# Kernel tuning notes

Hardware: AMD Instinct MI355X
Metric: run time of the kernel (lower is better)

Reference implementation:

```python
import jax, jax.numpy as jnp
import numpy as np

B, T = 16, 64
IN, H = 256, 512          # input_size, hidden_size (= output_size)
M, W, R = 256, 64, 4      # nr_cells, cell_size, read_heads
NN_IN = R * W + IN        # controller input size = 512
IFACE = R * W + 3 * W + 5 * R + 3  # 471
DELTA = 1e-6


def _lin(key, fan_out, fan_in):
    k1, k2 = jax.random.split(key)
    s = 1.0 / np.sqrt(fan_in)
    Wm = jax.random.uniform(k1, (fan_out, fan_in), minval=-s, maxval=s, dtype=jnp.float32)
    b = jax.random.uniform(k2, (fan_out,), minval=-s, maxval=s, dtype=jnp.float32)
    return Wm, b


def setup_inputs() -> dict:
    key = jax.random.key(0)
    ks = jax.random.split(key, 8)
    x = jax.random.normal(ks[0], (B, T, IN), dtype=jnp.float32)
    Wih0, bih0 = _lin(ks[1], 4 * H, NN_IN)
    Whh0, bhh0 = _lin(ks[2], 4 * H, H)
    Wih1, bih1 = _lin(ks[3], 4 * H, H)
    Whh1, bhh1 = _lin(ks[4], 4 * H, H)
    Wout, bout = _lin(ks[5], H, H)              # output_weights
    Wif, bif = _lin(ks[6], IFACE, H)            # memory interface_weights
    Wmem, bmem = _lin(ks[7], IN, R * W + H)     # mem_out
    return dict(x=x, Wih0=Wih0, bih0=bih0, Whh0=Whh0, bhh0=bhh0,
                Wih1=Wih1, bih1=bih1, Whh1=Whh1, bhh1=bhh1,
                Wout=Wout, bout=bout, Wif=Wif, bif=bif, Wmem=Wmem, bmem=bmem)


def _lstm(x, h, c, Wih, bih, Whh, bhh):
    g = x @ Wih.T + bih + h @ Whh.T + bhh
    i, f, gg, o = jnp.split(g, 4, axis=-1)  # torch LSTMCell gate order i,f,g,o
    i, f, o = jax.nn.sigmoid(i), jax.nn.sigmoid(f), jax.nn.sigmoid(o)
    c = f * c + i * jnp.tanh(gg)
    return o * jnp.tanh(c), c


def _content_weights(mem, keys, strengths):
    # mem (B,M,W), keys (B,K,W), strengths (B,K) -> softmax cosine weights (B,K,M)
    mn = mem / (jnp.linalg.norm(mem, axis=2, keepdims=True) + DELTA)
    kn = keys / (jnp.linalg.norm(keys, axis=2, keepdims=True) + DELTA)
    sim = jnp.einsum('bkw,bmw->bkm', kn, mn)
    return jax.nn.softmax(sim * strengths[:, :, None], axis=2)


def _dnc_forward(x, Wih0, bih0, Whh0, bhh0, Wih1, bih1, Whh1, bhh1,
                 Wout, bout, Wif, bif, Wmem, bmem):
    Bz, Tz = x.shape[0], x.shape[1]
    eye_mask = 1.0 - jnp.eye(M, dtype=x.dtype)
    # NOTE: in the source, last_read (zeros at init) is concatenated to EVERY
    # timestep's input and never updated inside the layer time loop.
    last_read = jnp.zeros((Bz, Tz, R * W), dtype=x.dtype)
    xs = jnp.swapaxes(jnp.concatenate([x, last_read], axis=-1), 0, 1)  # (T,B,NN_IN)

    def step(carry, xt):
        h0, c0, h1, c1, mem, link, prec, rw, ww, usage = carry
        h0, c0 = _lstm(xt, h0, c0, Wih0, bih0, Whh0, bhh0)
        h1, c1 = _lstm(h0, h1, c1, Wih1, bih1, Whh1, bhh1)
        out = h1 @ Wout.T + bout
        xi = h1 @ Wif.T + bif  # (B, IFACE)
        o1 = R * W
        rk = jnp.tanh(xi[:, :o1]).reshape(Bz, R, W)
        rs = jax.nn.softplus(xi[:, o1:o1 + R])
        o2 = o1 + R
        wk = jnp.tanh(xi[:, o2:o2 + W]).reshape(Bz, 1, W)
        ws = jax.nn.softplus(xi[:, o2 + W:o2 + W + 1])          # (B,1)
        ev = jax.nn.sigmoid(xi[:, o2 + W + 1:o2 + 2 * W + 1])   # erase (B,W)
        wv = jnp.tanh(xi[:, o2 + 2 * W + 1:o2 + 3 * W + 1])     # write vec (B,W)
        o3 = o2 + 3 * W + 1
        fg = jax.nn.sigmoid(xi[:, o3:o3 + R])                   # free gates (B,R)
        ag = jax.nn.sigmoid(xi[:, o3 + R:o3 + R + 1])           # alloc gate (B,1)
        wg = jax.nn.sigmoid(xi[:, o3 + R + 1:o3 + R + 2])       # write gate (B,1)
        rm = jax.nn.softmax(xi[:, o3 + R + 2:].reshape(Bz, R, 3), axis=-1)
        # --- usage update (single write head: 1 - prod(1-ww) == ww) ---
        usage = usage + (1.0 - usage) * ww
        psi = jnp.prod(1.0 - fg[:, :, None] * rw, axis=1)
        usage = usage * psi
        # --- write content weighting ---
        wcw = _content_weights(mem, wk, ws)[:, 0]  # (B,M)
        # --- allocation via sort + exclusive cumprod + inverse scatter ---
        u = DELTA + (1.0 - DELTA) * usage
        idx = jnp.argsort(u, axis=1)  # ascending usage = free list
        su = jnp.take_along_axis(u, idx, axis=1)
        prod_excl = jnp.cumprod(jnp.concatenate([jnp.ones((Bz, 1), u.dtype), su], 1), axis=1)[:, :-1]
        sa = (1.0 - su) * prod_excl
        alloc = jnp.take_along_axis(sa, jnp.argsort(idx, axis=1), axis=1)  # (B,M)
        # --- write weighting ---
        ww = wg * (ag * alloc + (1.0 - ag) * wcw)  # (B,M)
        # --- memory erase + write ---
        mem = mem * (1.0 - ww[:, :, None] * ev[:, None, :]) + ww[:, :, None] * wv[:, None, :]
        # --- temporal link matrix (diag zeroed) + precedence ---
        link = (1.0 - ww[:, :, None] - ww[:, None, :]) * link + ww[:, :, None] * prec[:, None, :]
        link = link * eye_mask
        prec = (1.0 - jnp.sum(ww, axis=1, keepdims=True)) * prec + ww
        # --- read: content + forward/backward directional modes ---
        cw = _content_weights(mem, rk, rs)            # (B,R,M)
        fwd = jnp.einsum('bmn,brn->brm', link, rw)    # L @ rw_prev
        bwd = jnp.einsum('brm,bmn->brn', rw, link)    # rw_prev @ L
        rw = rm[:, :, 0:1] * bwd + rm[:, :, 1:2] * fwd + rm[:, :, 2:3] * cw
        read_vecs = jnp.einsum('brm,bmw->brw', rw, mem).reshape(Bz, R * W)
        y = jnp.concatenate([out, read_vecs], axis=1) @ Wmem.T + bmem  # mem_out, dropout=0
        return (h0, c0, h1, c1, mem, link, prec, rw, ww, usage), y

    z = lambda *s: jnp.zeros(s, dtype=x.dtype)
    init = (z(Bz, H), z(Bz, H), z(Bz, H), z(Bz, H),
            z(Bz, M, W), z(Bz, M, M), z(Bz, M), z(Bz, R, M), z(Bz, M), z(Bz, M))
    _, ys = jax.lax.scan(step, init, xs)
    return jnp.swapaxes(ys, 0, 1)  # (B,T,IN)


def reference(x, Wih0, bih0, Whh0, bhh0, Wih1, bih1, Whh1, bhh1,
              Wout, bout, Wif, bif, Wmem, bmem):
    return _dnc_forward(x, Wih0, bih0, Whh0, bhh0, Wih1, bih1, Whh1, bhh1,
                        Wout, bout, Wif, bif, Wmem, bmem)
```

## Files before the change

kernel.cpp:

```cpp
#include <hip/hip_runtime.h>
#include <math.h>


#define BZ    16
#define TZ    64
#define HID   512
#define NCELL 256
#define CSZ   64
#define NRD   4
#define G4H   2048
#define IFC   471
#define DEL   1e-6f
#define SMT   257
#define NLSTM 192
#define NTOT  224

__device__ __forceinline__ float sig_(float x) { return 1.f / (1.f + expf(-x)); }
__device__ __forceinline__ float splus_(float x) { return fmaxf(x, 0.f) + log1pf(expf(-fabsf(x))); }

template <int SLP>
__device__ __forceinline__ unsigned poll_acq(unsigned* ptr, unsigned tgt) {
  unsigned v;
  while ((v = __hip_atomic_load(ptr, __ATOMIC_RELAXED, __HIP_MEMORY_SCOPE_AGENT)) < tgt)
    __builtin_amdgcn_s_sleep(SLP);
  v = __hip_atomic_load(ptr, __ATOMIC_ACQUIRE, __HIP_MEMORY_SCOPE_AGENT);
  return v;
}

__global__ __launch_bounds__(256) void k_transpose(const float* __restrict__ src,
                                                   float* __restrict__ dst,
                                                   int rows, int cols, int kmax, int dst_stride) {
  __shared__ float tile[32][33];
  int c0 = blockIdx.x * 32, r0 = blockIdx.y * 32;
  int tx = threadIdx.x, ty = threadIdx.y;
  for (int i = ty; i < 32; i += 8) {
    int r = r0 + i, c = c0 + tx;
    tile[i][tx] = (r < rows && c < cols) ? src[(size_t)r * cols + c] : 0.f;
  }
  __syncthreads();
  for (int i = ty; i < 32; i += 8) {
    int c = c0 + i, r = r0 + tx;
    if (c < kmax && r < rows) dst[(size_t)c * dst_stride + r] = tile[tx][i];
  }
}

__global__ __launch_bounds__(256) void k_xpart(const float* __restrict__ x,
                                               const float* __restrict__ Wih0T,
                                               const float* __restrict__ bih0,
                                               const float* __restrict__ bhh0,
                                               float* __restrict__ xpart) {
  const int lane = threadIdx.x, ty = threadIdx.y;
  const int jg = blockIdx.x * 64 + lane;
  const int tb0 = blockIdx.y * 16;
  __shared__ float sx[16][256];
  const int tid = ty * 64 + lane;
  for (int idx = tid; idx < 16 * 256; idx += 256) {
    int row = idx >> 8, k = idx & 255;
    int tb = tb0 + row, tt = tb >> 4, bb = tb & 15;
    sx[row][k] = x[((size_t)bb * TZ + tt) * 256 + k];
  }
  __syncthreads();
  float acc[4] = {0.f, 0.f, 0.f, 0.f};
  for (int k = 0; k < 256; ++k) {
    float wv = Wih0T[(size_t)k * G4H + jg];
#pragma unroll
    for (int i = 0; i < 4; ++i) acc[i] = fmaf(wv, sx[ty * 4 + i][k], acc[i]);
  }
  float bias = bih0[jg] + bhh0[jg];
#pragma unroll
  for (int i = 0; i < 4; ++i)
    xpart[(size_t)(tb0 + ty * 4 + i) * G4H + jg] = acc[i] + bias;
}

__device__ __forceinline__ void gbar(unsigned* done, unsigned* go,
                                     unsigned tgt, int bid, int tid) {
  __syncthreads();
  if (bid == 0) {
    if (tid == 0)
      __hip_atomic_store(&done[0], tgt, __ATOMIC_RELEASE, __HIP_MEMORY_SCOPE_AGENT);
    if (tid < NLSTM) (void)poll_acq<4>(&done[tid], tgt);
    __syncthreads();
    if (tid == 0)
      __hip_atomic_store(go, tgt, __ATOMIC_RELEASE, __HIP_MEMORY_SCOPE_AGENT);
  } else {
    if (tid == 0) {
      __hip_atomic_store(&done[bid], tgt, __ATOMIC_RELEASE, __HIP_MEMORY_SCOPE_AGENT);
      (void)poll_acq<4>(go, tgt);
    }
    __syncthreads();
  }
}

#define SCR(s, i) scr[(s) * 1320 + (i)]

__global__ __launch_bounds__(1024, 1) void k_fused(
    const float* __restrict__ xpart,
    const float* __restrict__ Whh0,
    const float* __restrict__ Wih1, const float* __restrict__ Whh1,
    const float* __restrict__ bih1, const float* __restrict__ bhh1,
    const float* __restrict__ WifT, const float* __restrict__ bif,
    float* __restrict__ h0g, float* __restrict__ h1g,
    float* __restrict__ h1_all, float* __restrict__ xi_all,
    float* __restrict__ linkg, float* __restrict__ rv_all,
    unsigned* __restrict__ done, unsigned* __restrict__ go,
    unsigned* __restrict__ xiflag) {
  const int tid = threadIdx.x;
  const int bid = blockIdx.x;
  __shared__ __align__(16) float SMEM[37264];

  if (bid < 64) {
    float* w0 = SMEM;
    float* hl = SMEM + 16768;
    float* sc = hl + 8320;
    float* xpl = sc + 4096;
    float* c0l = xpl + 512;
    const int j0 = bid * 8;
    for (int lr = 0; lr < 32; ++lr) {
      int g = lr >> 3, jj2 = lr & 7;
      const float* src = Whh0 + (size_t)(g * 512 + j0 + jj2) * 512;
      for (int k = tid; k < 512; k += 1024) w0[lr * 524 + k] = src[k];
    }
    if (tid < 128) c0l[tid] = 0.f;
    const int ks = tid & 7, bq = (tid >> 3) & 3, jj = tid >> 5;
    const int wr0 = (0 * 8 + (jj & 7)) * 524, wr1 = (1 * 8 + (jj & 7)) * 524,
              wr2 = (2 * 8 + (jj & 7)) * 524, wr3 = (3 * 8 + (jj & 7)) * 524;
    const int hb0 = (bq * 4 + 0) * 520, hb1 = (bq * 4 + 1) * 520,
              hb2 = (bq * 4 + 2) * 520, hb3 = (bq * 4 + 3) * 520;
    for (int ph = 0; ph < 65; ++ph) {
      if (ph < 64) {
        const int t = ph, po = t & 1, pn = po ^ 1;
        for (int q = tid; q < 2048; q += 1024) {
          int bb = q >> 7, kq = q & 127;
          ((float4*)&hl[bb * 520])[kq] = ((const float4*)&h0g[(size_t)(po * 16 + bb) * 512])[kq];
        }
        if (tid < 512) {
          int bb = tid >> 5, g = (tid >> 3) & 3, j2 = tid & 7;
          xpl[tid] = xpart[((size_t)t * 16 + bb) * G4H + g * 512 + j0 + j2];
        }
        __syncthreads();
        if (tid < 256) {
          float4 a0 = {0,0,0,0}, a1 = {0,0,0,0}, a2 = {0,0,0,0}, a3 = {0,0,0,0};
#pragma unroll 4
          for (int i = 0; i < 16; ++i) {
            const int off = ks * 4 + 32 * i;
            float4 w4a = *(const float4*)&w0[wr0 + off];
            float4 w4b = *(const float4*)&w0[wr1 + off];
            float4 w4c = *(const float4*)&w0[wr2 + off];
            float4 w4d = *(const float4*)&w0[wr3 + off];
            float4 h4a = *(const float4*)&hl[hb0 + off];
            float4 h4b = *(const float4*)&hl[hb1 + off];
            float4 h4c = *(const float4*)&hl[hb2 + off];
            float4 h4d = *(const float4*)&hl[hb3 + off];
            a0.x += w4a.x*h4a.x + w4a.y*h4a.y + w4a.z*h4a.z + w4a.w*h4a.w;
            a0.y += w4a.x*h4b.x + w4a.y*h4b.y + w4a.z*h4b.z + w4a.w*h4b.w;
            a0.z += w4a.x*h4c.x + w4a.y*h4c.y + w4a.z*h4c.z + w4a.w*h4c.w;
            a0.w += w4a.x*h4d.x + w4a.y*h4d.y + w4a.z*h4d.z + w4a.w*h4d.w;
            a1.x += w4b.x*h4a.x + w4b.y*h4a.y + w4b.z*h4a.z + w4b.w*h4a.w;
            a1.y += w4b.x*h4b.x + w4b.y*h4b.y + w4b.z*h4b.z + w4b.w*h4b.w;
            a1.z += w4b.x*h4c.x + w4b.y*h4c.y + w4b.z*h4c.z + w4b.w*h4c.w;
            a1.w += w4b.x*h4d.x + w4b.y*h4d.y + w4b.z*h4d.z + w4b.w*h4d.w;
            a2.x += w4c.x*h4a.x + w4c.y*h4a.y + w4c.z*h4a.z + w4c.w*h4a.w;
            a2.y += w4c.x*h4b.x + w4c.y*h4b.y + w4c.z*h4b.z + w4c.w*h4b.w;
            a2.z += w4c.x*h4c.x + w4c.y*h4c.y + w4c.z*h4c.z + w4c.w*h4c.w;
            a2.w += w4c.x*h4d.x + w4c.y*h4d.y + w4c.z*h4d.z + w4c.w*h4d.w;
            a3.x += w4d.x*h4a.x + w4d.y*h4a.y + w4d.z*h4a.z + w4d.w*h4a.w;
            a3.y += w4d.x*h4b.x + w4d.y*h4b.y + w4d.z*h4b.z + w4d.w*h4b.w;
            a3.z += w4d.x*h4c.x + w4d.y*h4c.y + w4d.z*h4c.z + w4d.w*h4c.w;
            a3.w += w4d.x*h4d.x + w4d.y*h4d.y + w4d.z*h4d.z + w4d.w*h4d.w;
          }
          *(float4*)&sc[ks * 512 + (0 * 8 + jj) * 16 + bq * 4] = a0;
          *(float4*)&sc[ks * 512 + (1 * 8 + jj) * 16 + bq * 4] = a1;
          *(float4*)&sc[ks * 512 + (2 * 8 + jj) * 16 + bq * 4] = a2;
          *(float4*)&sc[ks * 512 + (3 * 8 + jj) * 16 + bq * 4] = a3;
        }
        __syncthreads();
        if (tid < 128) {
          const int bb = tid >> 3, j2 = tid & 7;
          float gs[4];
#pragma unroll
          for (int g = 0; g < 4; ++g) {
            float s = 0.f;
#pragma unroll
            for (int k2 = 0; k2 < 8; ++k2) s += sc[k2 * 512 + (g * 8 + j2) * 16 + bb];
            gs[g] = s + xpl[bb * 32 + g * 8 + j2];
          }
          float gi = sig_(gs[0]), gf = sig_(gs[1]), gg = tanhf(gs[2]), go_ = sig_(gs[3]);
          float cc = gf * c0l[j2 * 16 + bb] + gi * gg;
          c0l[j2 * 16 + bb] = cc;
          h0g[(size_t)(pn * 16 + bb) * 512 + j0 + j2] = go_ * tanhf(cc);
        }
      }
      gbar(done, go, (unsigned)(ph + 1), bid, tid);
    }
  } else if (bid < 192) {
    float* w1 = SMEM;
    float* h0l = SMEM + 16448;
    float* h1l = h0l + 8320;
    float* sc = h1l + 8320;
    float* c1l = sc + 4096;
    float* bl = c1l + 64;
    const int b1 = bid - 64;
    const int j0 = b1 * 4;
    for (int lr = 0; lr < 16; ++lr) {
      int g = lr >> 2, jj2 = lr & 3;
      const float* si = Wih1 + (size_t)(g * 512 + j0 + jj2) * 512;
      const float* sh = Whh1 + (size_t)(g * 512 + j0 + jj2) * 512;
      for (int k = tid; k < 512; k += 1024) {
        w1[lr * 1028 + k] = si[k];
        w1[lr * 1028 + 512 + k] = sh[k];
      }
    }
    if (tid < 64) c1l[tid] = 0.f;
    if (tid < 16) {
      int g = tid >> 2, jj2 = tid & 3;
      bl[tid] = bih1[g * 512 + j0 + jj2] + bhh1[g * 512 + j0 + jj2];
    }
    const int ks = tid & 15, bq = (tid >> 4) & 3, jj = (tid >> 6) & 3;
    const int wr0 = (0 * 4 + jj) * 1028, wr1 = (1 * 4 + jj) * 1028,
              wr2 = (2 * 4 + jj) * 1028, wr3 = (3 * 4 + jj) * 1028;
    const int hb0 = (bq * 4 + 0) * 520, hb1 = (bq * 4 + 1) * 520,
              hb2 = (bq * 4 + 2) * 520, hb3 = (bq * 4 + 3) * 520;
    for (int ph = 0; ph < 65; ++ph) {
      if (ph >= 1) {
        const int t = ph - 1, po = t & 1, pn = po ^ 1;
        for (int q = tid; q < 2048; q += 1024) {
          int bb = q >> 7, kq = q & 127;
          ((float4*)&h0l[bb * 520])[kq] = ((const float4*)&h0g[(size_t)(pn * 16 + bb) * 512])[kq];
          ((float4*)&h1l[bb * 520])[kq] = ((const float4*)&h1g[(size_t)(po * 16 + bb) * 512])[kq];
        }
        __syncthreads();
        if (tid < 256) {
          float4 a0 = {0,0,0,0}, a1 = {0,0,0,0}, a2 = {0,0,0,0}, a3 = {0,0,0,0};
#pragma unroll 4
          for (int i = 0; i < 16; ++i) {
            const int offw = ks * 4 + 64 * i;
            const int offh = (i < 8) ? offw : (offw - 512);
            const float* hsrc = (i < 8) ? h0l : h1l;
            float4 w4a = *(const float4*)&w1[wr0 + offw];
            float4 w4b = *(const float4*)&w1[wr1 + offw];
            float4 w4c = *(const float4*)&w1[wr2 + offw];
            float4 w4d = *(const float4*)&w1[wr3 + offw];
            float4 h4a = *(const float4*)&hsrc[hb0 + offh];
            float4 h4b = *(const float4*)&hsrc[hb1 + offh];
            float4 h4c = *(const float4*)&hsrc[hb2 + offh];
            float4 h4d = *(const float4*)&hsrc[hb3 + offh];
            a0.x += w4a.x*h4a.x + w4a.y*h4a.y + w4a.z*h4a.z + w4a.w*h4a.w;
            a0.y += w4a.x*h4b.x + w4a.y*h4b.y + w4a.z*h4b.z + w4a.w*h4b.w;
            a0.z += w4a.x*h4c.x + w4a.y*h4c.y + w4a.z*h4c.z + w4a.w*h4c.w;
            a0.w += w4a.x*h4d.x + w4a.y*h4d.y + w4a.z*h4d.z + w4a.w*h4d.w;
            a1.x += w4b.x*h4a.x + w4b.y*h4a.y + w4b.z*h4a.z + w4b.w*h4a.w;
            a1.y += w4b.x*h4b.x + w4b.y*h4b.y + w4b.z*h4b.z + w4b.w*h4b.w;
            a1.z += w4b.x*h4c.x + w4b.y*h4c.y + w4b.z*h4c.z + w4b.w*h4c.w;
            a1.w += w4b.x*h4d.x + w4b.y*h4d.y + w4b.z*h4d.z + w4b.w*h4d.w;
            a2.x += w4c.x*h4a.x + w4c.y*h4a.y + w4c.z*h4a.z + w4c.w*h4a.w;
            a2.y += w4c.x*h4b.x + w4c.y*h4b.y + w4c.z*h4b.z + w4c.w*h4b.w;
            a2.z += w4c.x*h4c.x + w4c.y*h4c.y + w4c.z*h4c.z + w4c.w*h4c.w;
            a2.w += w4c.x*h4d.x + w4c.y*h4d.y + w4c.z*h4d.z + w4c.w*h4d.w;
            a3.x += w4d.x*h4a.x + w4d.y*h4a.y + w4d.z*h4a.z + w4d.w*h4a.w;
            a3.y += w4d.x*h4b.x + w4d.y*h4b.y + w4d.z*h4b.z + w4d.w*h4b.w;
            a3.z += w4d.x*h4c.x + w4d.y*h4c.y + w4d.z*h4c.z + w4d.w*h4c.w;
            a3.w += w4d.x*h4d.x + w4d.y*h4d.y + w4d.z*h4d.z + w4d.w*h4d.w;
          }
          *(float4*)&sc[ks * 256 + (0 * 4 + jj) * 16 + bq * 4] = a0;
          *(float4*)&sc[ks * 256 + (1 * 4 + jj) * 16 + bq * 4] = a1;
          *(float4*)&sc[ks * 256 + (2 * 4 + jj) * 16 + bq * 4] = a2;
          *(float4*)&sc[ks * 256 + (3 * 4 + jj) * 16 + bq * 4] = a3;
        }
        __syncthreads();
        if (tid < 64) {
          const int bb = tid >> 2, j2 = tid & 3;
          float gs[4];
#pragma unroll
          for (int g = 0; g < 4; ++g) {
            float s = 0.f;
#pragma unroll
            for (int k2 = 0; k2 < 16; ++k2) s += sc[k2 * 256 + (g * 4 + j2) * 16 + bb];
            gs[g] = s + bl[g * 4 + j2];
          }
          float gi = sig_(gs[0]), gf = sig_(gs[1]), gg = tanhf(gs[2]), go_ = sig_(gs[3]);
          float cc = gf * c1l[j2 * 16 + bb] + gi * gg;
          c1l[j2 * 16 + bb] = cc;
          float hv = go_ * tanhf(cc);
          h1g[(size_t)(pn * 16 + bb) * 512 + j0 + j2] = hv;
          h1_all[((size_t)t * 16 + bb) * 512 + j0 + j2] = hv;
        }
      }
      gbar(done, go, (unsigned)(ph + 1), bid, tid);
    }
  } else if (bid < 208) {
    const int b = bid - 192;
    float* sh1 = SMEM;
    float* sxo = SMEM + 512;
    __shared__ unsigned sgo;
    unsigned seen_go = 0;
    for (int t = 0; t < TZ; ++t) {
      if (tid == 0 && seen_go < (unsigned)(t + 2)) {
        sgo = poll_acq<8>(go, (unsigned)(t + 2));
      }
      __syncthreads();
      seen_go = (sgo > seen_go) ? sgo : seen_go;
      if (tid < 512) sh1[tid] = h1_all[((size_t)t * BZ + b) * HID + tid];
      __syncthreads();
      {
        const int u = tid & 511, half = tid >> 9;
        if (u < IFC) {
          const float* wc = WifT + u;
          const int k0 = half * 256;
          float acc = 0.f;
#pragma unroll 8
          for (int k = k0; k < k0 + 256; ++k)
            acc = fmaf(sh1[k], wc[(size_t)k * 512], acc);
          sxo[half * 512 + u] = acc;
        }
      }
      __syncthreads();
      if (tid < IFC)
        xi_all[((size_t)t * BZ + b) * 512 + tid] = sxo[tid] + sxo[512 + tid] + bif[tid];
      __syncthreads();
      if (tid == 0)
        __hip_atomic_store(&xiflag[b], (unsigned)(t + 1), __ATOMIC_RELEASE, __HIP_MEMORY_SCOPE_AGENT);
    }
  } else {
    const int b = bid - 208;
    const int lane = tid & 63;
    const int wv = tid >> 6;
    const int m8 = tid & 255;
    const int seg = tid >> 8;
    float* LNK = linkg + (size_t)b * (NCELL * NCELL);

    float* smemT = SMEM;
    float* sxi   = smemT + 16448;
    float* srkn  = sxi + 472;
    float* swkn  = srkn + 256;
    float* sev   = swkn + 64;
    float* swvv  = sev + 64;
    float* sscal = swvv + 64;
    float* srw   = sscal + 40;
    float* sww   = srw + 1024;
    float* susage = sww + 256;
    float* sprec = susage + 256;
    float* ssim  = sprec + 256;
    float* sfwd  = ssim + 1024;
    float* sbwd  = sfwd + 1024;
    float* sa    = sbwd + 1056;
    float* sc_   = sa + 256;
    float* sb_   = sc_ + 256;
    int*   srank = (int*)(sb_ + 256);
    float* scr   = (float*)(srank + 256);
    float* sred2 = scr + 5280;
    __shared__ unsigned sflag;

    for (int i = tid; i < CSZ * SMT; i += 1024) smemT[i] = 0.f;
    if (tid < 256) {
      sww[tid] = 0.f; susage[tid] = 0.f; sprec[tid] = 0.f;
      srw[tid] = 0.f; srw[256 + tid] = 0.f; srw[512 + tid] = 0.f; srw[768 + tid] = 0.f;
    }
    for (int i = tid; i < (NCELL * NCELL) / 4; i += 1024)
      ((float4*)LNK)[i] = make_float4(0.f, 0.f, 0.f, 0.f);
    __syncthreads();

    unsigned seen = 0;
    for (int t = 0; t < TZ; ++t) {
      if (tid == 0 && seen < (unsigned)(t + 1)) {
        sflag = poll_acq<8>(&xiflag[b], (unsigned)(t + 1));
      }
      __syncthreads();
      if (seen < (unsigned)(t + 1)) seen = sflag;

      if (tid < IFC) sxi[tid] = xi_all[((size_t)t * BZ + b) * 512 + tid];
      __syncthreads();
      if (wv < 4) {
        float v = tanhf(sxi[wv * 64 + lane]);
        float s2 = v * v;
#pragma unroll
        for (int off = 32; off; off >>= 1) s2 += __shfl_xor(s2, off);
        srkn[wv * 64 + lane] = v / (sqrtf(s2) + DEL);
      } else if (wv == 4) {
        float v = tanhf(sxi[260 + lane]);
        float s2 = v * v;
#pragma unroll
        for (int off = 32; off; off >>= 1) s2 += __shfl_xor(s2, off);
        swkn[lane] = v / (sqrtf(s2) + DEL);
      } else if (wv == 5) {
        sev[lane] = sig_(sxi[325 + lane]);
      } else if (wv == 6) {
        swvv[lane] = tanhf(sxi[389 + lane]);
      } else if (wv == 7) {
        if (lane < 4) sscal[lane] = splus_(sxi[256 + lane]);
        if (lane == 4) sscal[4] = splus_(sxi[324]);
        if (lane >= 8 && lane < 12) sscal[lane] = sig_(sxi[453 + (lane - 8)]);
        if (lane == 12) sscal[12] = sig_(sxi[457]);
        if (lane == 13) sscal[13] = sig_(sxi[458]);
        if (lane >= 16 && lane < 20) {
          int r = lane - 16;
          float a = sxi[459 + r * 3], b2 = sxi[460 + r * 3], c2 = sxi[461 + r * 3];
          float mx3 = fmaxf(a, fmaxf(b2, c2));
          float ea = expf(a - mx3), eb = expf(b2 - mx3), ec = expf(c2 - mx3);
          float iv = 1.f / (ea + eb + ec);
          sscal[20 + r * 3 + 0] = ea * iv;
          sscal[20 + r * 3 + 1] = eb * iv;
          sscal[20 + r * 3 + 2] = ec * iv;
        }
      }
      __syncthreads();

      float un_r = 0.f;
      if (tid < 256) {
        float wwo = sww[tid], uo = susage[tid];
        float u1 = uo + (1.f - uo) * wwo;
        float psi = 1.f;
#pragma unroll
        for (int r = 0; r < 4; ++r) psi *= 1.f - sscal[8 + r] * srw[r * 256 + tid];
        un_r = u1 * psi;
        susage[tid] = un_r;
      }
      {
        float dot = 0.f, nn = 0.f;
#pragma unroll 4
        for (int w = seg * 16; w < seg * 16 + 16; ++w) {
          float mv = smemT[w * SMT + m8];
          dot = fmaf(mv, swkn[w], dot);
          nn = fmaf(mv, mv, nn);
        }
        SCR(seg, 0 * 264 + m8) = dot;
        SCR(seg, 1 * 264 + m8) = nn;
      }
      __syncthreads();
      float e_r = 0.f, simv = 0.f;
      if (tid < 256) {
        float dot = SCR(0, tid) + SCR(1, tid) + SCR(2, tid) + SCR(3, tid);
        float nn = SCR(0, 264 + tid) + SCR(1, 264 + tid) + SCR(2, 264 + tid) + SCR(3, 264 + tid);
        simv = sscal[4] * dot / (sqrtf(nn) + DEL);
        float mx = simv;
#pragma unroll
        for (int off = 32; off; off >>= 1) mx = fmaxf(mx, __shfl_xor(mx, off));
        if (lane == 0) sred2[wv] = mx;
      }
      __syncthreads();
      if (tid < 256) {
        float mx = fmaxf(fmaxf(sred2[0], sred2[1]), fmaxf(sred2[2], sred2[3]));
        e_r = expf(simv - mx);
        float s = e_r;
#pragma unroll
        for (int off = 32; off; off >>= 1) s += __shfl_xor(s, off);
        if (lane == 0) sred2[8 + wv] = s;
      }
      __syncthreads();
      float wcw_r = 0.f;
      if (tid < 256) {
        float sm = sred2[8] + sred2[9] + sred2[10] + sred2[11];
        wcw_r = e_r / sm;
        sa[tid] = DEL + (1.f - DEL) * un_r;
      }
      __syncthreads();

      {
        float um = sa[m8];
        int cnt = 0;
        for (int j2 = seg * 64; j2 < seg * 64 + 64; ++j2) {
          float uj = sa[j2];
          cnt += (uj < um || (uj == um && j2 < m8)) ? 1 : 0;
        }
        ((int*)&SCR(seg, 0))[m8] = cnt;
      }
      __syncthreads();
      if (tid < 256) {
        int rank = ((int*)&SCR(0, 0))[tid] + ((int*)&SCR(1, 0))[tid] +
                   ((int*)&SCR(2, 0))[tid] + ((int*)&SCR(3, 0))[tid];
        srank[tid] = rank;
        sb_[rank] = sa[tid];
      }
      __syncthreads();
      float inc = 0.f;
      if (tid < 256) {
        inc = sb_[tid];
#pragma unroll
        for (int off = 1; off < 64; off <<= 1) {
          float pp = __shfl_up(inc, off);
          if (lane >= off) inc *= pp;
        }
        if (lane == 63) sred2[16 + wv] = inc;
      }
      __syncthreads();
      if (tid < 256) {
        float pref = 1.f;
        for (int w2 = 0; w2 < wv; ++w2) pref *= sred2[16 + w2];
        float excl = __shfl_up(inc, 1);
        if (lane == 0) excl = 1.f;
        sc_[tid] = excl * pref;
      }
      __syncthreads();

      if (tid < 256) {
        float alo = (1.f - sa[tid]) * sc_[srank[tid]];
        float wwn = sscal[13] * (sscal[12] * alo + (1.f - sscal[12]) * wcw_r);
        sww[tid] = wwn;
        float s = wwn;
#pragma unroll
        for (int off = 32; off; off >>= 1) s += __shfl_xor(s, off);
        if (lane == 0) sred2[24 + wv] = s;
      }
      __syncthreads();
      if (tid == 0) sscal[14] = sred2[24] + sred2[25] + sred2[26] + sred2[27];

      {
        float wm = sww[m8];
        float nn = 0.f, d0 = 0.f, d1 = 0.f, d2 = 0.f, d3 = 0.f;
#pragma unroll 4
        for (int w = seg * 16; w < seg * 16 + 16; ++w) {
          float v = smemT[w * SMT + m8];
          v = v * (1.f - wm * sev[w]) + wm * swvv[w];
          smemT[w * SMT + m8] = v;
          nn = fmaf(v, v, nn);
          d0 = fmaf(v, srkn[0 * 64 + w], d0);
          d1 = fmaf(v, srkn[1 * 64 + w], d1);
          d2 = fmaf(v, srkn[2 * 64 + w], d2);
          d3 = fmaf(v, srkn[3 * 64 + w], d3);
        }
        SCR(seg, 0 * 264 + m8) = nn;
        SCR(seg, 1 * 264 + m8) = d0;
        SCR(seg, 2 * 264 + m8) = d1;
        SCR(seg, 3 * 264 + m8) = d2;
        SCR(seg, 4 * 264 + m8) = d3;
      }
      for (int i = tid; i < NRD * 264; i += 1024) sbwd[i] = 0.f;
      __syncthreads();
      float sv0 = 0.f, sv1 = 0.f, sv2 = 0.f, sv3 = 0.f;
      float e0 = 0.f, e1 = 0.f, e2 = 0.f, e3 = 0.f;
      if (tid < 256) {
        float nn = SCR(0, tid) + SCR(1, tid) + SCR(2, tid) + SCR(3, tid);
        float invn = 1.f / (sqrtf(nn) + DEL);
        sv0 = sscal[0] * (SCR(0, 264 + tid) + SCR(1, 264 + tid) + SCR(2, 264 + tid) + SCR(3, 264 + tid)) * invn;
        sv1 = sscal[1] * (SCR(0, 528 + tid) + SCR(1, 528 + tid) + SCR(2, 528 + tid) + SCR(3, 528 + tid)) * invn;
        sv2 = sscal[2] * (SCR(0, 792 + tid) + SCR(1, 792 + tid) + SCR(2, 792 + tid) + SCR(3, 792 + tid)) * invn;
        sv3 = sscal[3] * (SCR(0, 1056 + tid) + SCR(1, 1056 + tid) + SCR(2, 1056 + tid) + SCR(3, 1056 + tid)) * invn;
        float m0 = sv0, m1 = sv1, m2 = sv2, m3 = sv3;
#pragma unroll
        for (int off = 32; off; off >>= 1) {
          m0 = fmaxf(m0, __shfl_xor(m0, off));
          m1 = fmaxf(m1, __shfl_xor(m1, off));
          m2 = fmaxf(m2, __shfl_xor(m2, off));
          m3 = fmaxf(m3, __shfl_xor(m3, off));
        }
        if (lane == 0) {
          sred2[wv * 4 + 0] = m0; sred2[wv * 4 + 1] = m1;
          sred2[wv * 4 + 2] = m2; sred2[wv * 4 + 3] = m3;
        }
      }
      __syncthreads();
      if (tid < 256) {
        float m0 = fmaxf(fmaxf(sred2[0], sred2[4]), fmaxf(sred2[8], sred2[12]));
        float m1 = fmaxf(fmaxf(sred2[1], sred2[5]), fmaxf(sred2[9], sred2[13]));
        float m2 = fmaxf(fmaxf(sred2[2], sred2[6]), fmaxf(sred2[10], sred2[14]));
        float m3 = fmaxf(fmaxf(sred2[3], sred2[7]), fmaxf(sred2[11], sred2[15]));
        e0 = expf(sv0 - m0); e1 = expf(sv1 - m1); e2 = expf(sv2 - m2); e3 = expf(sv3 - m3);
        float s0 = e0, s1 = e1, s2 = e2, s3 = e3;
#pragma unroll
        for (int off = 32; off; off >>= 1) {
          s0 += __shfl_xor(s0, off); s1 += __shfl_xor(s1, off);
          s2 += __shfl_xor(s2, off); s3 += __shfl_xor(s3, off);
        }
        if (lane == 0) {
          sred2[32 + wv * 4 + 0] = s0; sred2[32 + wv * 4 + 1] = s1;
          sred2[32 + wv * 4 + 2] = s2; sred2[32 + wv * 4 + 3] = s3;
        }
      }
      __syncthreads();
      if (tid < 256) {
        float s0 = sred2[32] + sred2[36] + sred2[40] + sred2[44];
        float s1 = sred2[33] + sred2[37] + sred2[41] + sred2[45];
        float s2 = sred2[34] + sred2[38] + sred2[42] + sred2[46];
        float s3 = sred2[35] + sred2[39] + sred2[43] + sred2[47];
        ssim[0 * 256 + tid] = e0 / s0; ssim[1 * 256 + tid] = e1 / s1;
        ssim[2 * 256 + tid] = e2 / s2; ssim[3 * 256 + tid] = e3 / s3;
      }

      {
        const float4 r0 = ((const float4*)(srw + 0 * 256))[lane];
        const float4 r1 = ((const float4*)(srw + 1 * 256))[lane];
        const float4 r2 = ((const float4*)(srw + 2 * 256))[lane];
        const float4 r3 = ((const float4*)(srw + 3 * 256))[lane];
        const float4 wc = ((const float4*)sww)[lane];
        const float4 pc = ((const float4*)sprec)[lane];
        const int n0 = lane * 4;
        float4 bp0 = {0,0,0,0}, bp1 = {0,0,0,0}, bp2 = {0,0,0,0}, bp3 = {0,0,0,0};
        for (int rr = 0; rr < 16; ++rr) {
          const int m = wv * 16 + rr;
          const float wm = sww[m];
          float4 lv = ((float4*)(LNK + (size_t)m * 256))[lane];
          lv.x = (1.f - wm - wc.x) * lv.x + wm * pc.x;
          lv.y = (1.f - wm - wc.y) * lv.y + wm * pc.y;
          lv.z = (1.f - wm - wc.z) * lv.z + wm * pc.z;
          lv.w = (1.f - wm - wc.w) * lv.w + wm * pc.w;
          if (m == n0 + 0) lv.x = 0.f;
          if (m == n0 + 1) lv.y = 0.f;
          if (m == n0 + 2) lv.z = 0.f;
          if (m == n0 + 3) lv.w = 0.f;
          ((float4*)(LNK + (size_t)m * 256))[lane] = lv;
          float f0 = lv.x * r0.x + lv.y * r0.y + lv.z * r0.z + lv.w * r0.w;
          float f1 = lv.x * r1.x + lv.y * r1.y + lv.z * r1.z + lv.w * r1.w;
          float f2 = lv.x * r2.x + lv.y * r2.y + lv.z * r2.z + lv.w * r2.w;
          float f3 = lv.x * r3.x + lv.y * r3.y + lv.z * r3.z + lv.w * r3.w;
#pragma unroll
          for (int off = 32; off; off >>= 1) {
            f0 += __shfl_xor(f0, off); f1 += __shfl_xor(f1, off);
            f2 += __shfl_xor(f2, off); f3 += __shfl_xor(f3, off);
          }
          if (lane == 0) {
            sfwd[0 * 256 + m] = f0; sfwd[1 * 256 + m] = f1;
            sfwd[2 * 256 + m] = f2; sfwd[3 * 256 + m] = f3;
          }
          const float s0 = srw[0 * 256 + m], s1 = srw[1 * 256 + m],
                      s2 = srw[2 * 256 + m], s3 = srw[3 * 256 + m];
          bp0.x = fmaf(lv.x, s0, bp0.x); bp0.y = fmaf(lv.y, s0, bp0.y);
          bp0.z = fmaf(lv.z, s0, bp0.z); bp0.w = fmaf(lv.w, s0, bp0.w);
          bp1.x = fmaf(lv.x, s1, bp1.x); bp1.y = fmaf(lv.y, s1, bp1.y);
          bp1.z = fmaf(lv.z, s1, bp1.z); bp1.w = fmaf(lv.w, s1, bp1.w);
          bp2.x = fmaf(lv.x, s2, bp2.x); bp2.y = fmaf(lv.y, s2, bp2.y);
          bp2.z = fmaf(lv.z, s2, bp2.z); bp2.w = fmaf(lv.w, s2, bp2.w);
          bp3.x = fmaf(lv.x, s3, bp3.x); bp3.y = fmaf(lv.y, s3, bp3.y);
          bp3.z = fmaf(lv.z, s3, bp3.z); bp3.w = fmaf(lv.w, s3, bp3.w);
        }
        atomicAdd(&sbwd[0 * 264 + n0 + 0], bp0.x); atomicAdd(&sbwd[0 * 264 + n0 + 1], bp0.y);
        atomicAdd(&sbwd[0 * 264 + n0 + 2], bp0.z); atomicAdd(&sbwd[0 * 264 + n0 + 3], bp0.w);
        atomicAdd(&sbwd[1 * 264 + n0 + 0], bp1.x); atomicAdd(&sbwd[1 * 264 + n0 + 1], bp1.y);
        atomicAdd(&sbwd[1 * 264 + n0 + 2], bp1.z); atomicAdd(&sbwd[1 * 264 + n0 + 3], bp1.w);
        atomicAdd(&sbwd[2 * 264 + n0 + 0], bp2.x); atomicAdd(&sbwd[2 * 264 + n0 + 1], bp2.y);
        atomicAdd(&sbwd[2 * 264 + n0 + 2], bp2.z); atomicAdd(&sbwd[2 * 264 + n0 + 3], bp2.w);
        atomicAdd(&sbwd[3 * 264 + n0 + 0], bp3.x); atomicAdd(&sbwd[3 * 264 + n0 + 1], bp3.y);
        atomicAdd(&sbwd[3 * 264 + n0 + 2], bp3.z); atomicAdd(&sbwd[3 * 264 + n0 + 3], bp3.w);
      }
      __syncthreads();

      if (tid < 256) {
#pragma unroll
        for (int r = 0; r < 4; ++r) {
          float rwn = sscal[20 + r * 3 + 0] * sbwd[r * 264 + tid] +
                      sscal[20 + r * 3 + 1] * sfwd[r * 256 + tid] +
                      sscal[20 + r * 3 + 2] * ssim[r * 256 + tid];
          srw[r * 256 + tid] = rwn;
        }
        sprec[tid] = (1.f - sscal[14]) * sprec[tid] + sww[tid];
      }
      __syncthreads();

      {
        const int r = tid >> 8, sg = (tid >> 6) & 3, w = lane;
        float acc = 0.f;
#pragma unroll 4
        for (int m2 = sg * 64; m2 < sg * 64 + 64; ++m2)
          acc = fmaf(srw[r * 256 + m2], smemT[w * SMT + m2], acc);
        SCR(sg, r * 64 + w) = acc;
      }
      __syncthreads();
      if (tid < 256)
        rv_all[((size_t)t * BZ + b) * 256 + tid] =
            SCR(0, tid) + SCR(1, tid) + SCR(2, tid) + SCR(3, tid);
      __syncthreads();
    }
  }
}

__global__ __launch_bounds__(256) void k_out(const float* __restrict__ h1_all,
                                             const float* __restrict__ WoutT,
                                             const float* __restrict__ bout,
                                             float* __restrict__ out_all) {
  const int lane = threadIdx.x, ty = threadIdx.y;
  const int u = blockIdx.x * 64 + lane;
  const int row0 = blockIdx.y * 16;
  __shared__ float sh[16][512];
  const int tid = ty * 64 + lane;
  for (int idx = tid; idx < 16 * 512; idx += 256) {
    int r2 = idx >> 9, k = idx & 511;
    sh[r2][k] = h1_all[(size_t)(row0 + r2) * 512 + k];
  }
  __syncthreads();
  const float* wcol = WoutT + u;
  float bias = bout[u];
  float acc[4] = {0.f, 0.f, 0.f, 0.f};
  for (int k = 0; k < 512; ++k) {
    float wv = wcol[(size_t)k * 512];
#pragma unroll
    for (int i = 0; i < 4; ++i) acc[i] = fmaf(wv, sh[ty * 4 + i][k], acc[i]);
  }
#pragma unroll
  for (int i = 0; i < 4; ++i)
    out_all[(size_t)(row0 + ty * 4 + i) * 512 + u] = acc[i] + bias;
}

__global__ __launch_bounds__(256) void k_y(const float* __restrict__ out_all,
                                           const float* __restrict__ rv_all,
                                           const float* __restrict__ WmemT,
                                           const float* __restrict__ bmem,
                                           float* __restrict__ y) {
  const int lane = threadIdx.x, ty = threadIdx.y;
  const int o = blockIdx.x * 64 + lane;
  const int tb0 = blockIdx.y * 16;
  __shared__ float sin_[16][768];
  const int tid = ty * 64 + lane;
  for (int idx = tid; idx < 16 * 768; idx += 256) {
    int row = idx / 768, k = idx % 768;
    int tb = tb0 + row;
    sin_[row][k] = (k < 512) ? out_all[(size_t)tb * HID + k]
                             : rv_all[(size_t)tb * 256 + (k - 512)];
  }
  __syncthreads();
  float acc[4] = {0.f, 0.f, 0.f, 0.f};
  for (int k = 0; k < 768; ++k) {
    float wv = WmemT[(size_t)k * 256 + o];
#pragma unroll
    for (int i = 0; i < 4; ++i) acc[i] = fmaf(wv, sin_[ty * 4 + i][k], acc[i]);
  }
  float bo = bmem[o];
#pragma unroll
  for (int i = 0; i < 4; ++i) {
    int tb = tb0 + ty * 4 + i;
    int tt = tb >> 4, bb = tb & 15;
    y[((size_t)bb * TZ + tt) * 256 + o] = acc[i] + bo;
  }
}

extern "C" void kernel_launch(void* const* d_in, const int* in_sizes, int n_in,
                              void* d_out, int out_size, void* d_ws, size_t ws_size,
                              hipStream_t stream) {
  (void)in_sizes; (void)n_in; (void)out_size; (void)ws_size;
  const float* x    = (const float*)d_in[0];
  const float* Wih0 = (const float*)d_in[1];
  const float* bih0 = (const float*)d_in[2];
  const float* Whh0 = (const float*)d_in[3];
  const float* bhh0 = (const float*)d_in[4];
  const float* Wih1 = (const float*)d_in[5];
  const float* bih1 = (const float*)d_in[6];
  const float* Whh1 = (const float*)d_in[7];
  const float* bhh1 = (const float*)d_in[8];
  const float* Wout = (const float*)d_in[9];
  const float* bout = (const float*)d_in[10];
  const float* Wif  = (const float*)d_in[11];
  const float* bif  = (const float*)d_in[12];
  const float* Wmem = (const float*)d_in[13];
  const float* bmem = (const float*)d_in[14];
  float* y = (float*)d_out;

  float* p = (float*)d_ws;
  auto take = [&](size_t n) { float* q = p; p += n; return q; };
  float* Wih0T   = take((size_t)256 * 2048);
  float* WoutT   = take((size_t)512 * 512);
  float* WifT    = take((size_t)512 * 512);
  float* WmemT   = take((size_t)768 * 256);
  float* xpart   = take((size_t)TZ * BZ * G4H);
  float* h1_all  = take((size_t)TZ * BZ * HID);
  float* out_all = take((size_t)TZ * BZ * HID);
  float* xi_all  = take((size_t)TZ * BZ * 512);
  float* rv_all  = take((size_t)TZ * BZ * 256);
  float* linkg   = take((size_t)BZ * NCELL * NCELL);
  float* zstart  = p;
  float* h0g     = take((size_t)2 * BZ * HID);
  float* h1g     = take((size_t)2 * BZ * HID);
  float* cntf    = take((size_t)512);
  size_t zbytes = (size_t)((char*)p - (char*)zstart);
  unsigned* done   = (unsigned*)cntf;
  unsigned* go     = done + 256;
  unsigned* xiflag = done + 320;

  (void)hipMemsetAsync(zstart, 0, zbytes, stream);

  dim3 tb32(32, 8);
  hipLaunchKernelGGL(k_transpose, dim3(8, 64), tb32, 0, stream, Wih0, Wih0T, 2048, 512, 256, 2048);
  hipLaunchKernelGGL(k_transpose, dim3(16, 16), tb32, 0, stream, Wout, WoutT, 512, 512, 512, 512);
  hipLaunchKernelGGL(k_transpose, dim3(16, 15), tb32, 0, stream, Wif, WifT, 471, 512, 512, 512);
  hipLaunchKernelGGL(k_transpose, dim3(24, 8), tb32, 0, stream, Wmem, WmemT, 256, 768, 768, 256);

  hipLaunchKernelGGL(k_xpart, dim3(32, 64), dim3(64, 4), 0, stream, x, Wih0T, bih0, bhh0, xpart);

  hipLaunchKernelGGL(k_fused, dim3(NTOT), dim3(1024), 0, stream,
                     xpart, Whh0, Wih1, Whh1, bih1, bhh1, WifT, bif,
                     h0g, h1g, h1_all, xi_all, linkg, rv_all, done, go, xiflag);

  hipLaunchKernelGGL(k_out, dim3(8, 64), dim3(64, 4), 0, stream, h1_all, WoutT, bout, out_all);

  hipLaunchKernelGGL(k_y, dim3(4, 64), dim3(64, 4), 0, stream, out_all, rv_all, WmemT, bmem, y);
}
```

Baseline: 3.975 ms.

## Remap fused kernel blocks to XCD-aware roles and batch interface projection

```diff
diff --git a/kernel.cpp b/kernel.cpp
--- a/kernel.cpp
+++ b/kernel.cpp
@@ -13,7 +13,6 @@
 #define DEL   1e-6f
 #define SMT   257
 #define NLSTM 192
-#define NTOT  224
 
 __device__ __forceinline__ float sig_(float x) { return 1.f / (1.f + expf(-x)); }
 __device__ __forceinline__ float splus_(float x) { return fmaxf(x, 0.f) + log1pf(expf(-fabsf(x))); }
@@ -73,18 +72,23 @@
 }
 
 __device__ __forceinline__ void gbar(unsigned* done, unsigned* go,
-                                     unsigned tgt, int bid, int tid) {
+                                     unsigned tgt, int r, int tid) {
   __syncthreads();
-  if (bid == 0) {
+  if (r == 0) {
     if (tid == 0)
       __hip_atomic_store(&done[0], tgt, __ATOMIC_RELEASE, __HIP_MEMORY_SCOPE_AGENT);
-    if (tid < NLSTM) (void)poll_acq<4>(&done[tid], tgt);
+    if (tid < NLSTM) {
+      while (__hip_atomic_load(&done[tid], __ATOMIC_RELAXED, __HIP_MEMORY_SCOPE_AGENT) < tgt)
+        __builtin_amdgcn_s_sleep(4);
+    }
     __syncthreads();
-    if (tid == 0)
+    if (tid == 0) {
+      __builtin_amdgcn_fence(__ATOMIC_ACQUIRE, "agent");
       __hip_atomic_store(go, tgt, __ATOMIC_RELEASE, __HIP_MEMORY_SCOPE_AGENT);
+    }
   } else {
     if (tid == 0) {
-      __hip_atomic_store(&done[bid], tgt, __ATOMIC_RELEASE, __HIP_MEMORY_SCOPE_AGENT);
+      __hip_atomic_store(&done[r], tgt, __ATOMIC_RELEASE, __HIP_MEMORY_SCOPE_AGENT);
       (void)poll_acq<4>(go, tgt);
     }
     __syncthreads();
@@ -106,15 +110,29 @@
     unsigned* __restrict__ xiflag) {
   const int tid = threadIdx.x;
   const int bid = blockIdx.x;
+  const int res = bid & 7;
+  const int gq = (bid >> 3) & 15;
+  int role, idx = 0;
+  if (res >= 2) {
+    int r = (bid >> 3) * 6 + (res - 2);
+    role = (r < 64) ? 0 : 1;
+    idx = r;
+  } else if (bid < 128) {
+    if ((gq & 1) == res) { role = 3; idx = gq; } else { role = 4; }
+  } else {
+    if ((gq & 1) != res) { role = 2; idx = gq; } else { role = 4; }
+  }
+  if (role == 4) return;
   __shared__ __align__(16) float SMEM[37264];
 
-  if (bid < 64) {
+  if (role == 0) {
     float* w0 = SMEM;
     float* hl = SMEM + 16768;
     float* sc = hl + 8320;
     float* xpl = sc + 4096;
     float* c0l = xpl + 512;
-    const int j0 = bid * 8;
+    const int rnk = idx;
+    const int j0 = rnk * 8;
     for (int lr = 0; lr < 32; ++lr) {
       int g = lr >> 3, jj2 = lr & 7;
       const float* src = Whh0 + (size_t)(g * 512 + j0 + jj2) * 512;
@@ -190,17 +208,17 @@
           h0g[(size_t)(pn * 16 + bb) * 512 + j0 + j2] = go_ * tanhf(cc);
         }
       }
-      gbar(done, go, (unsigned)(ph + 1), bid, tid);
-    }
-  } else if (bid < 192) {
+      gbar(done, go, (unsigned)(ph + 1), rnk, tid);
+    }
+  } else if (role == 1) {
     float* w1 = SMEM;
     float* h0l = SMEM + 16448;
     float* h1l = h0l + 8320;
     float* sc = h1l + 8320;
     float* c1l = sc + 4096;
     float* bl = c1l + 64;
-    const int b1 = bid - 64;
-    const int j0 = b1 * 4;
+    const int rnk = idx;
+    const int j0 = (rnk - 64) * 4;
     for (int lr = 0; lr < 16; ++lr) {
       int g = lr >> 2, jj2 = lr & 3;
       const float* si = Wih1 + (size_t)(g * 512 + j0 + jj2) * 512;
@@ -285,43 +303,47 @@
           h1_all[((size_t)t * 16 + bb) * 512 + j0 + j2] = hv;
         }
       }
-      gbar(done, go, (unsigned)(ph + 1), bid, tid);
-    }
-  } else if (bid < 208) {
-    const int b = bid - 192;
+      gbar(done, go, (unsigned)(ph + 1), rnk, tid);
+    }
+  } else if (role == 2) {
+    const int b = idx;
     float* sh1 = SMEM;
     float* sxo = SMEM + 512;
     __shared__ unsigned sgo;
     unsigned seen_go = 0;
-    for (int t = 0; t < TZ; ++t) {
-      if (tid == 0 && seen_go < (unsigned)(t + 2)) {
-        sgo = poll_acq<8>(go, (unsigned)(t + 2));
-      }
-      __syncthreads();
-      seen_go = (sgo > seen_go) ? sgo : seen_go;
-      if (tid < 512) sh1[tid] = h1_all[((size_t)t * BZ + b) * HID + tid];
-      __syncthreads();
-      {
-        const int u = tid & 511, half = tid >> 9;
-        if (u < IFC) {
-          const float* wc = WifT + u;
-          const int k0 = half * 256;
-          float acc = 0.f;
+    for (int tc = 0; tc < TZ / 4; ++tc) {
+      const unsigned need = (unsigned)(4 * tc + 5);
+      if (tid == 0 && seen_go < need) {
+        sgo = poll_acq<8>(go, need);
+      }
+      __syncthreads();
+      if (seen_go < need) seen_go = sgo;
+      for (int k4 = 0; k4 < 4; ++k4) {
+        const int t = 4 * tc + k4;
+        if (tid < 512) sh1[tid] = h1_all[((size_t)t * BZ + b) * HID + tid];
+        __syncthreads();
+        {
+          const int u = tid & 511, half = tid >> 9;
+          if (u < IFC) {
+            const float* wc = WifT + u;
+            const int k0 = half * 256;
+            float acc = 0.f;
 #pragma unroll 8
-          for (int k = k0; k < k0 + 256; ++k)
-            acc = fmaf(sh1[k], wc[(size_t)k * 512], acc);
-          sxo[half * 512 + u] = acc;
-        }
-      }
-      __syncthreads();
-      if (tid < IFC)
-        xi_all[((size_t)t * BZ + b) * 512 + tid] = sxo[tid] + sxo[512 + tid] + bif[tid];
-      __syncthreads();
+            for (int k = k0; k < k0 + 256; ++k)
+              acc = fmaf(sh1[k], wc[(size_t)k * 512], acc);
+            sxo[half * 512 + u] = acc;
+          }
+        }
+        __syncthreads();
+        if (tid < IFC)
+          xi_all[((size_t)t * BZ + b) * 512 + tid] = sxo[tid] + sxo[512 + tid] + bif[tid];
+        __syncthreads();
+      }
       if (tid == 0)
-        __hip_atomic_store(&xiflag[b], (unsigned)(t + 1), __ATOMIC_RELEASE, __HIP_MEMORY_SCOPE_AGENT);
+        __hip_atomic_store(&xiflag[b], (unsigned)(4 * tc + 4), __ATOMIC_RELEASE, __HIP_MEMORY_SCOPE_AGENT);
     }
   } else {
-    const int b = bid - 208;
+    const int b = idx;
     const int lane = tid & 63;
     const int wv = tid >> 6;
     const int m8 = tid & 255;
@@ -772,7 +794,7 @@
 
   hipLaunchKernelGGL(k_xpart, dim3(32, 64), dim3(64, 4), 0, stream, x, Wih0T, bih0, bhh0, xpart);
 
-  hipLaunchKernelGGL(k_fused, dim3(NTOT), dim3(1024), 0, stream,
+  hipLaunchKernelGGL(k_fused, dim3(256), dim3(1024), 0, stream,
                      xpart, Whh0, Wih1, Whh1, bih1, bhh1, WifT, bif,
                      h0g, h1g, h1_all, xi_all, linkg, rv_all, done, go, xiflag);
 
```

New measurement: 3.819 ms. 1.04x faster.
